# Kernel optimization log

Hardware: AMD Instinct MI355X
Metric: run time of the kernel (lower is better)

The kernel has to match this reference:

```python
import jax, jax.numpy as jnp
import numpy as np

K = 32          # neighbors
HEAD_DIM = 8    # out_channels // num_heads = 64 // 8


def _ln(x, g, b, eps=1e-5):
    m = x.mean(-1, keepdims=True)
    v = ((x - m) ** 2).mean(-1, keepdims=True)
    return (x - m) * jax.lax.rsqrt(v + eps) * g + b


def _knn(x, k):
    # x: [B,N,3]; torch code takes top-k of NEGATIVE squared distance -> nearest
    sq = jnp.sum(x * x, axis=-1)                        # [B,N]
    inner = jnp.einsum('bnc,bmc->bnm', x, x)            # [B,N,N]
    neg_dist = -(sq[:, :, None] - 2.0 * inner + sq[:, None, :])
    return jax.lax.top_k(neg_dist, k)[1]                # [B,N,k]


def _gather(points, idx):
    # points: [B,M,C], idx: [B,N,K] -> [B,N,K,C]
    return jax.vmap(lambda p, i: p[i])(points, idx)


def _forward(xyz, features, ln1_g, ln1_b, Wq, bq, Wk, bk, Wv, bv,
             d_W1, d_b1, d_g, d_b, d_W2, d_b2,
             g_W1, g_b1, g_g, g_b, g_W2, g_b2,
             Wo, bo, ln2_g, ln2_b, ca_W1, ca_b1, ca_W2, ca_b2, ln3_g, ln3_b):
    fn = _ln(features, ln1_g, ln1_b)                    # norm1
    idx = _knn(xyz, K)                                  # [B,N,K]
    nxyz = _gather(xyz, idx)                            # [B,N,K,3]
    nfeat = _gather(fn, idx)                            # [B,N,K,C]
    pos_diff = xyz[:, :, None, :] - nxyz                # [B,N,K,3]
    # fc_delta: Linear -> LN -> ReLU -> Linear
    pe = jax.nn.relu(_ln(pos_diff @ d_W1 + d_b1, d_g, d_b)) @ d_W2 + d_b2
    q = (fn @ Wq + bq)[:, :, None, :]                   # [B,N,1,C]
    k = nfeat @ Wk + bk                                 # [B,N,K,C]
    v = nfeat @ Wv + bv
    # head permutes in torch are identity reshapes; vector attention in [B,N,K,C]
    attn_in = q - k + pe
    a = jax.nn.relu(_ln(attn_in @ g_W1 + g_b1, g_g, g_b)) @ g_W2 + g_b2
    a = jax.nn.softmax(a / np.sqrt(HEAD_DIM).astype(np.float32), axis=2)
    out = jnp.sum(a * (v + pe), axis=2)                 # [B,N,C]
    out = _ln(out @ Wo + bo, ln2_g, ln2_b)              # fc_out + norm2
    cw = jax.nn.sigmoid(jax.nn.relu(out.mean(axis=1) @ ca_W1 + ca_b1) @ ca_W2 + ca_b2)
    out = _ln(out * cw[:, None, :], ln3_g, ln3_b)       # channel attn + norm3
    return out + features                               # in==out -> no skip_proj


def setup_inputs() -> dict:
    key = jax.random.key(0)
    ks = jax.random.split(key, 12)
    B, N, C = 2, 8192, 64
    s = 1.0 / np.sqrt(C)
    w = lambda k, shape, sc: jax.random.normal(k, shape, jnp.float32) * sc
    return dict(
        xyz=jax.random.normal(ks[0], (B, N, 3), jnp.float32),
        features=jax.random.normal(ks[1], (B, N, C), jnp.float32),
        ln1_g=jnp.ones(C), ln1_b=jnp.zeros(C),
        Wq=w(ks[2], (C, C), s), bq=jnp.zeros(C),
        Wk=w(ks[3], (C, C), s), bk=jnp.zeros(C),
        Wv=w(ks[4], (C, C), s), bv=jnp.zeros(C),
        d_W1=w(ks[5], (3, C), 1.0 / np.sqrt(3)), d_b1=jnp.zeros(C),
        d_g=jnp.ones(C), d_b=jnp.zeros(C),
        d_W2=w(ks[6], (C, C), s), d_b2=jnp.zeros(C),
        g_W1=w(ks[7], (C, C), s), g_b1=jnp.zeros(C),
        g_g=jnp.ones(C), g_b=jnp.zeros(C),
        g_W2=w(ks[8], (C, C), s), g_b2=jnp.zeros(C),
        Wo=w(ks[9], (C, C), s), bo=jnp.zeros(C),
        ln2_g=jnp.ones(C), ln2_b=jnp.zeros(C),
        ca_W1=w(ks[10], (C, C // 4), s), ca_b1=jnp.zeros(C // 4),
        ca_W2=w(ks[11], (C // 4, C), 1.0 / np.sqrt(C // 4)), ca_b2=jnp.zeros(C),
        ln3_g=jnp.ones(C), ln3_b=jnp.zeros(C),
    )


def reference(xyz, features, ln1_g, ln1_b, Wq, bq, Wk, bk, Wv, bv,
              d_W1, d_b1, d_g, d_b, d_W2, d_b2,
              g_W1, g_b1, g_g, g_b, g_W2, g_b2,
              Wo, bo, ln2_g, ln2_b, ca_W1, ca_b1, ca_W2, ca_b2, ln3_g, ln3_b):
    return _forward(xyz, features, ln1_g, ln1_b, Wq, bq, Wk, bk, Wv, bv,
                    d_W1, d_b1, d_g, d_b, d_W2, d_b2,
                    g_W1, g_b1, g_g, g_b, g_W2, g_b2,
                    Wo, bo, ln2_g, ln2_b, ca_W1, ca_b1, ca_W2, ca_b2, ln3_g, ln3_b)
```

## Files before the change

### kernel.cpp

```cpp
#include <hip/hip_runtime.h>

static constexpr int gB = 2;
static constexpr int gN = 8192;
static constexpr int gC = 64;
static constexpr int gK = 32;

using u16 = unsigned short;
using u32 = unsigned int;
using u64 = unsigned long long;

__device__ __forceinline__ float wsum(float v) {
#pragma unroll
    for (int m = 32; m; m >>= 1) v += __shfl_xor(v, m, 64);
    return v;
}

__device__ __forceinline__ u16 f2bf(float f) {
    u32 u = __float_as_uint(f);
    return (u16)((u + 0x7FFFu + ((u >> 16) & 1u)) >> 16);
}
__device__ __forceinline__ float bf2f(u16 v) {
    return __uint_as_float(((u32)v) << 16);
}

__global__ __launch_bounds__(256) void k_lnqkv(
    const float* __restrict__ feat, const float* __restrict__ ln1g, const float* __restrict__ ln1b,
    const float* __restrict__ Wq, const float* __restrict__ bq,
    const float* __restrict__ Wk, const float* __restrict__ bk,
    const float* __restrict__ Wv, const float* __restrict__ bv,
    float* __restrict__ Qo, float* __restrict__ Ko, float* __restrict__ Vo,
    float* __restrict__ zero_region)
{
    if (blockIdx.x == 0) zero_region[threadIdx.x] = 0.f;
    int wave = threadIdx.x >> 6, lane = threadIdx.x & 63;
    int p = blockIdx.x * 4 + wave;
    float x = feat[(size_t)p * gC + lane];
    float mu = wsum(x) * (1.f / 64);
    float d = x - mu;
    float var = wsum(d * d) * (1.f / 64);
    float inv = 1.f / sqrtf(var + 1e-5f);
    float fn = d * inv * ln1g[lane] + ln1b[lane];
    float qa = bq[lane], ka = bk[lane], va = bv[lane];
    for (int cp = 0; cp < 64; ++cp) {
        float hv = __shfl(fn, cp, 64);
        qa += hv * Wq[cp * 64 + lane];
        ka += hv * Wk[cp * 64 + lane];
        va += hv * Wv[cp * 64 + lane];
    }
    size_t o = (size_t)p * gC + lane;
    Qo[o] = qa; Ko[o] = ka; Vo[o] = va;
}

__global__ __launch_bounds__(256) void k_pack(const float* __restrict__ xyz,
                                              float4* __restrict__ pk4)
{
#pragma clang fp contract(off)
    int p = blockIdx.x * 256 + threadIdx.x;
    const float* s = xyz + (size_t)p * 3;
    float x = s[0], y = s[1], z = s[2];
    float n = sqrtf((x * x + y * y) + z * z);
    pk4[p] = make_float4(x, y, z, n * n);
}

__global__ __launch_bounds__(64) void k_knn(const float4* __restrict__ pk4, int* __restrict__ idxo)
{
#pragma clang fp contract(off)
    int lane = threadIdx.x;
    int q = blockIdx.x;
    int b = q >> 13;
    int n = q & (gN - 1);
    const float4* base = pk4 + (size_t)b * gN;
    float4 me = base[n];
    float xi = me.x, yi = me.y, zi = me.z;
    float sqi = me.w;
    u64 lst[10];
#pragma unroll
    for (int e = 0; e < 10; ++e) lst[e] = 0ull;
#pragma unroll 4
    for (int jj = 0; jj < 128; ++jj) {
        int j = (jj << 6) | lane;
        float4 c4 = base[j];
        float inner = (xi * c4.x + yi * c4.y) + zi * c4.z;
        float nd = -((sqi - 2.0f * inner) + c4.w);
        u32 u = __float_as_uint(nd);
        u32 kh = u ^ (0x80000000u | (u32)((int)u >> 31));
        u64 pk = ((u64)kh << 32) | (u32)(8191 - j);
        if (pk > lst[9]) {
            lst[9] = pk;
#pragma unroll
            for (int e = 9; e > 0; --e) {
                if (lst[e] > lst[e - 1]) { u64 t = lst[e - 1]; lst[e - 1] = lst[e]; lst[e] = t; }
            }
        }
    }
    int* op = idxo + (size_t)q * gK;
    for (int r = 0; r < gK; ++r) {
        u64 g = lst[0];
#pragma unroll
        for (int m = 32; m; m >>= 1) {
            u64 o = __shfl_xor(g, m, 64);
            g = (o > g) ? o : g;
        }
        if (lst[0] == g) {
#pragma unroll
            for (int e = 0; e < 9; ++e) lst[e] = lst[e + 1];
            lst[9] = 0ull;
        }
        if (lane == 0) op[r] = 8191 - (int)(g & 0x1FFFu);
    }
}

__global__ __launch_bounds__(256, 2) void k_attn(
    const float* __restrict__ xyz,
    const float* __restrict__ Qb, const float* __restrict__ Kb, const float* __restrict__ Vb,
    const int* __restrict__ idxi,
    const float* __restrict__ dW1, const float* __restrict__ db1,
    const float* __restrict__ dgv, const float* __restrict__ dbv,
    const float* __restrict__ dW2, const float* __restrict__ db2,
    const float* __restrict__ gW1, const float* __restrict__ gb1,
    const float* __restrict__ ggv, const float* __restrict__ gbv,
    const float* __restrict__ gW2, const float* __restrict__ gb2,
    float* __restrict__ att)
{
    __shared__ u16 wd2s[64 * 64];
    __shared__ u16 wg1s[64 * 64];
    __shared__ u16 wg2s[64 * 64];
    __shared__ float hbuf[4][32][64];
    __shared__ u16 pebuf[4][32][64];
    __shared__ float4 dxb[4][32];
    __shared__ int jb[4][32];

    int tid = threadIdx.x;
    int w = tid >> 6, lane = tid & 63;
    int p = blockIdx.x * 4 + w;
    int b = p >> 13;

    for (int i = tid; i < 4096; i += 256) {
        int cp = i >> 6, c = i & 63;
        int di = c * 64 + ((((cp >> 2) ^ (c & 15)) << 2) | (cp & 3));
        wd2s[di] = f2bf(dW2[i]);
        wg1s[di] = f2bf(gW1[i]);
        wg2s[di] = f2bf(gW2[i]);
    }
    if (lane < 32) {
        int j = idxi[(size_t)p * gK + lane];
        jb[w][lane] = j;
        const float* xp = xyz + (size_t)p * 3;
        const float* xj = xyz + ((size_t)b * gN + j) * 3;
        dxb[w][lane] = make_float4(xp[0] - xj[0], xp[1] - xj[1], xp[2] - xj[2], 0.f);
    }
    __syncthreads();

    float w1x = dW1[lane], w1y = dW1[64 + lane], w1z = dW1[128 + lane], vb1 = db1[lane];
    float vdg = dgv[lane], vdb = dbv[lane];
    float vb2 = db2[lane];
    float vg1b = gb1[lane], vgg = ggv[lane], vgb = gbv[lane], vg2b = gb2[lane];
    float q = Qb[(size_t)p * gC + lane];

#pragma unroll
    for (int kk = 0; kk < 32; ++kk) {
        float4 d4 = dxb[w][kk];
        float t = d4.x * w1x + d4.y * w1y + d4.z * w1z + vb1;
        float mu = wsum(t) * (1.f / 64);
        float td = t - mu;
        float var = wsum(td * td) * (1.f / 64);
        float inv = 1.f / sqrtf(var + 1e-5f);
        hbuf[w][kk][lane] = fmaxf(td * inv * vdg + vdb, 0.f);
    }

    float acc[32];

#pragma unroll
    for (int kk = 0; kk < 32; ++kk) acc[kk] = vb2;
    for (int cp4 = 0; cp4 < 16; ++cp4) {
        int pg = cp4 ^ (lane & 15);
        uint2 wp = *reinterpret_cast<const uint2*>(&wd2s[lane * 64 + pg * 4]);
        float w0 = bf2f((u16)(wp.x & 0xFFFFu)), w1 = bf2f((u16)(wp.x >> 16));
        float w2 = bf2f((u16)(wp.y & 0xFFFFu)), w3 = bf2f((u16)(wp.y >> 16));
#pragma unroll
        for (int kk = 0; kk < 32; ++kk) {
            float4 h4 = *reinterpret_cast<const float4*>(&hbuf[w][kk][cp4 * 4]);
            acc[kk] += h4.x * w0 + h4.y * w1 + h4.z * w2 + h4.w * w3;
        }
    }
#pragma unroll
    for (int kk = 0; kk < 32; ++kk) pebuf[w][kk][lane] = f2bf(acc[kk]);

    {
        const float* Kbb = Kb + (size_t)b * gN * gC;
#pragma unroll
        for (int kk = 0; kk < 32; ++kk) {
            float kv = Kbb[(size_t)jb[w][kk] * gC + lane];
            hbuf[w][kk][lane] = (q - kv) + acc[kk];
        }
    }

#pragma unroll
    for (int kk = 0; kk < 32; ++kk) acc[kk] = vg1b;
    for (int cp4 = 0; cp4 < 16; ++cp4) {
        int pg = cp4 ^ (lane & 15);
        uint2 wp = *reinterpret_cast<const uint2*>(&wg1s[lane * 64 + pg * 4]);
        float w0 = bf2f((u16)(wp.x & 0xFFFFu)), w1 = bf2f((u16)(wp.x >> 16));
        float w2 = bf2f((u16)(wp.y & 0xFFFFu)), w3 = bf2f((u16)(wp.y >> 16));
#pragma unroll
        for (int kk = 0; kk < 32; ++kk) {
            float4 h4 = *reinterpret_cast<const float4*>(&hbuf[w][kk][cp4 * 4]);
            acc[kk] += h4.x * w0 + h4.y * w1 + h4.z * w2 + h4.w * w3;
        }
    }
#pragma unroll
    for (int kk = 0; kk < 32; ++kk) {
        float a = acc[kk];
        float mu = wsum(a) * (1.f / 64);
        float ad = a - mu;
        float var = wsum(ad * ad) * (1.f / 64);
        float inv = 1.f / sqrtf(var + 1e-5f);
        hbuf[w][kk][lane] = fmaxf(ad * inv * vgg + vgb, 0.f);
    }

#pragma unroll
    for (int kk = 0; kk < 32; ++kk) acc[kk] = vg2b;
    for (int cp4 = 0; cp4 < 16; ++cp4) {
        int pg = cp4 ^ (lane & 15);
        uint2 wp = *reinterpret_cast<const uint2*>(&wg2s[lane * 64 + pg * 4]);
        float w0 = bf2f((u16)(wp.x & 0xFFFFu)), w1 = bf2f((u16)(wp.x >> 16));
        float w2 = bf2f((u16)(wp.y & 0xFFFFu)), w3 = bf2f((u16)(wp.y >> 16));
#pragma unroll
        for (int kk = 0; kk < 32; ++kk) {
            float4 h4 = *reinterpret_cast<const float4*>(&hbuf[w][kk][cp4 * 4]);
            acc[kk] += h4.x * w0 + h4.y * w1 + h4.z * w2 + h4.w * w3;
        }
    }

#pragma unroll
    for (int kk = 0; kk < 32; ++kk) acc[kk] *= 0.3535533905932738f;
    float mx = acc[0];
#pragma unroll
    for (int kk = 1; kk < 32; ++kk) mx = fmaxf(mx, acc[kk]);
    float s = 0.f;
#pragma unroll
    for (int kk = 0; kk < 32; ++kk) { acc[kk] = expf(acc[kk] - mx); s += acc[kk]; }
    {
        const float* Vbb = Vb + (size_t)b * gN * gC;
        float o = 0.f;
#pragma unroll
        for (int kk = 0; kk < 32; ++kk) {
            float vv = Vbb[(size_t)jb[w][kk] * gC + lane];
            o += acc[kk] * (vv + bf2f(pebuf[w][kk][lane]));
        }
        att[(size_t)p * gC + lane] = o / s;
    }
}

__global__ __launch_bounds__(256) void k_out(
    float* __restrict__ att,
    const float* __restrict__ Wo, const float* __restrict__ bo,
    const float* __restrict__ ln2g, const float* __restrict__ ln2b,
    float* __restrict__ meanb)
{
    __shared__ __align__(16) float hb[4][64];
    int lane = threadIdx.x & 63;
    int p = blockIdx.x * 4 + (threadIdx.x >> 6);
    int b = p >> 13;
    float* hbuf = hb[threadIdx.x >> 6];
    float wo[64];
#pragma unroll
    for (int r = 0; r < 64; ++r) wo[r] = Wo[r * 64 + lane];
    float x = att[(size_t)p * gC + lane];
    hbuf[lane] = x;
    float acc = bo[lane];
#pragma unroll
    for (int q4 = 0; q4 < 16; ++q4) {
        float4 hq = *reinterpret_cast<const float4*>(&hbuf[q4 * 4]);
        acc += hq.x * wo[q4 * 4 + 0] + hq.y * wo[q4 * 4 + 1]
             + hq.z * wo[q4 * 4 + 2] + hq.w * wo[q4 * 4 + 3];
    }
    float mu = wsum(acc) * (1.f / 64);
    float d = acc - mu;
    float var = wsum(d * d) * (1.f / 64);
    float inv = 1.f / sqrtf(var + 1e-5f);
    float y = d * inv * ln2g[lane] + ln2b[lane];
    att[(size_t)p * gC + lane] = y;
    atomicAdd(&meanb[b * 64 + lane], y * (1.f / gN));
}

__global__ void k_cw(const float* __restrict__ meanb,
                     const float* __restrict__ caW1, const float* __restrict__ cab1,
                     const float* __restrict__ caW2, const float* __restrict__ cab2,
                     float* __restrict__ cw)
{
    int b = blockIdx.x, lane = threadIdx.x;
    float mv = meanb[b * 64 + lane];
    float hj = (lane < 16) ? cab1[lane] : 0.f;
    for (int cp = 0; cp < 64; ++cp) {
        float mcp = __shfl(mv, cp, 64);
        if (lane < 16) hj += mcp * caW1[cp * 16 + lane];
    }
    hj = fmaxf(hj, 0.f);
    float acc = cab2[lane];
    for (int jj = 0; jj < 16; ++jj) {
        float hv = __shfl(hj, jj, 64);
        acc += hv * caW2[jj * 64 + lane];
    }
    cw[b * 64 + lane] = 1.f / (1.f + expf(-acc));
}

__global__ __launch_bounds__(256) void k_final(
    const float* __restrict__ out2, const float* __restrict__ cw,
    const float* __restrict__ ln3g, const float* __restrict__ ln3b,
    const float* __restrict__ feat, float* __restrict__ outp)
{
    int lane = threadIdx.x & 63;
    int p = blockIdx.x * 4 + (threadIdx.x >> 6);
    int b = p >> 13;
    float x = out2[(size_t)p * gC + lane] * cw[b * 64 + lane];
    float mu = wsum(x) * (1.f / 64);
    float d = x - mu;
    float var = wsum(d * d) * (1.f / 64);
    float inv = 1.f / sqrtf(var + 1e-5f);
    float y = d * inv * ln3g[lane] + ln3b[lane];
    outp[(size_t)p * gC + lane] = y + feat[(size_t)p * gC + lane];
}

extern "C" void kernel_launch(void* const* d_in, const int* in_sizes, int n_in,
                              void* d_out, int out_size, void* d_ws, size_t ws_size,
                              hipStream_t stream)
{
    (void)in_sizes; (void)n_in; (void)out_size; (void)ws_size;
    const float* xyz  = (const float*)d_in[0];
    const float* feat = (const float*)d_in[1];
    const float* ln1g = (const float*)d_in[2];
    const float* ln1b = (const float*)d_in[3];
    const float* Wq   = (const float*)d_in[4];
    const float* bq   = (const float*)d_in[5];
    const float* Wk   = (const float*)d_in[6];
    const float* bk   = (const float*)d_in[7];
    const float* Wv   = (const float*)d_in[8];
    const float* bv   = (const float*)d_in[9];
    const float* dW1  = (const float*)d_in[10];
    const float* db1  = (const float*)d_in[11];
    const float* dg   = (const float*)d_in[12];
    const float* db   = (const float*)d_in[13];
    const float* dW2  = (const float*)d_in[14];
    const float* db2  = (const float*)d_in[15];
    const float* gW1  = (const float*)d_in[16];
    const float* gb1  = (const float*)d_in[17];
    const float* gg   = (const float*)d_in[18];
    const float* gb   = (const float*)d_in[19];
    const float* gW2  = (const float*)d_in[20];
    const float* gb2  = (const float*)d_in[21];
    const float* Wo   = (const float*)d_in[22];
    const float* bo   = (const float*)d_in[23];
    const float* ln2g = (const float*)d_in[24];
    const float* ln2b = (const float*)d_in[25];
    const float* caW1 = (const float*)d_in[26];
    const float* cab1 = (const float*)d_in[27];
    const float* caW2 = (const float*)d_in[28];
    const float* cab2 = (const float*)d_in[29];
    const float* ln3g = (const float*)d_in[30];
    const float* ln3b = (const float*)d_in[31];

    const size_t BNC = (size_t)gB * gN * gC;
    float* Q    = (float*)d_ws;
    float* Kt   = Q + BNC;
    float* Vt   = Kt + BNC;
    float* att  = Vt + BNC;
    int*   idx  = (int*)(att + BNC);
    float* meanb = (float*)(idx + (size_t)gB * gN * gK);
    float* cw    = meanb + 128;
    float4* pk4  = (float4*)(cw + 128);

    const int PB = (gB * gN) / 4;

    k_lnqkv<<<PB, 256, 0, stream>>>(feat, ln1g, ln1b, Wq, bq, Wk, bk, Wv, bv, Q, Kt, Vt, meanb);
    k_pack<<<(gB * gN) / 256, 256, 0, stream>>>(xyz, pk4);
    k_knn<<<gB * gN, 64, 0, stream>>>(pk4, idx);
    k_attn<<<PB, 256, 0, stream>>>(xyz, Q, Kt, Vt, idx,
                                   dW1, db1, dg, db, dW2, db2,
                                   gW1, gb1, gg, gb, gW2, gb2, att);
    k_out<<<PB, 256, 0, stream>>>(att, Wo, bo, ln2g, ln2b, meanb);
    k_cw<<<gB, 64, 0, stream>>>(meanb, caW1, cab1, caW2, cab2, cw);
    k_final<<<PB, 256, 0, stream>>>(att, cw, ln3g, ln3b, feat, (float*)d_out);
}
```

Before: 1.067 ms.

## Share candidate point tiles in LDS across four queries per KNN block

The KNN kernel now processes four query points per 256-thread block and stages candidate coordinates into shared memory in 1024-point tiles (as SoA arrays). Each wave then reads candidates from LDS instead of loading them from global memory itself, cutting global and L2 traffic fourfold. In exchange it adds two block-wide barriers per tile, and waves whose top-k insertions diverge at different rates may stall one another at those barriers.

```diff
diff --git a/kernel.cpp b/kernel.cpp
--- a/kernel.cpp
+++ b/kernel.cpp
@@ -62,11 +62,13 @@
     pk4[p] = make_float4(x, y, z, n * n);
 }
 
-__global__ __launch_bounds__(64) void k_knn(const float4* __restrict__ pk4, int* __restrict__ idxo)
+__global__ __launch_bounds__(256) void k_knn(const float4* __restrict__ pk4, int* __restrict__ idxo)
 {
 #pragma clang fp contract(off)
-    int lane = threadIdx.x;
-    int q = blockIdx.x;
+    __shared__ float xs[1024], ys[1024], zs[1024], ws[1024];
+    int tid = threadIdx.x;
+    int wave = tid >> 6, lane = tid & 63;
+    int q = blockIdx.x * 4 + wave;
     int b = q >> 13;
     int n = q & (gN - 1);
     const float4* base = pk4 + (size_t)b * gN;
@@ -76,20 +78,31 @@
     u64 lst[10];
 #pragma unroll
     for (int e = 0; e < 10; ++e) lst[e] = 0ull;
+
+    for (int tile = 0; tile < 8; ++tile) {
+        __syncthreads();
+#pragma unroll
+        for (int t0 = 0; t0 < 4; ++t0) {
+            int t = tid + (t0 << 8);
+            float4 c = base[(tile << 10) + t];
+            xs[t] = c.x; ys[t] = c.y; zs[t] = c.z; ws[t] = c.w;
+        }
+        __syncthreads();
 #pragma unroll 4
-    for (int jj = 0; jj < 128; ++jj) {
-        int j = (jj << 6) | lane;
-        float4 c4 = base[j];
-        float inner = (xi * c4.x + yi * c4.y) + zi * c4.z;
-        float nd = -((sqi - 2.0f * inner) + c4.w);
-        u32 u = __float_as_uint(nd);
-        u32 kh = u ^ (0x80000000u | (u32)((int)u >> 31));
-        u64 pk = ((u64)kh << 32) | (u32)(8191 - j);
-        if (pk > lst[9]) {
-            lst[9] = pk;
-#pragma unroll
-            for (int e = 9; e > 0; --e) {
-                if (lst[e] > lst[e - 1]) { u64 t = lst[e - 1]; lst[e - 1] = lst[e]; lst[e] = t; }
+        for (int i = 0; i < 16; ++i) {
+            int t = (i << 6) | lane;
+            int j = (tile << 10) + t;
+            float inner = (xi * xs[t] + yi * ys[t]) + zi * zs[t];
+            float nd = -((sqi - 2.0f * inner) + ws[t]);
+            u32 u = __float_as_uint(nd);
+            u32 kh = u ^ (0x80000000u | (u32)((int)u >> 31));
+            u64 pk = ((u64)kh << 32) | (u32)(8191 - j);
+            if (pk > lst[9]) {
+                lst[9] = pk;
+#pragma unroll
+                for (int e = 9; e > 0; --e) {
+                    if (lst[e] > lst[e - 1]) { u64 tm = lst[e - 1]; lst[e - 1] = lst[e]; lst[e] = tm; }
+                }
             }
         }
     }
@@ -374,7 +387,7 @@
 
     k_lnqkv<<<PB, 256, 0, stream>>>(feat, ln1g, ln1b, Wq, bq, Wk, bk, Wv, bv, Q, Kt, Vt, meanb);
     k_pack<<<(gB * gN) / 256, 256, 0, stream>>>(xyz, pk4);
-    k_knn<<<gB * gN, 64, 0, stream>>>(pk4, idx);
+    k_knn<<<PB, 256, 0, stream>>>(pk4, idx);
     k_attn<<<PB, 256, 0, stream>>>(xyz, Q, Kt, Vt, idx,
                                    dW1, db1, dg, db, dW2, db2,
                                    gW1, gb1, gg, gb, gW2, gb2, att);
```

New measurement: 1.054 ms (median of 2 runs). Within noise of the previous version (-1.3%).
